# Kernel tuning notes

Measured on AMD Instinct MI355X. Metric: run time of the kernel, lower is better.

The kernel has to match this reference:

```python
import jax, jax.numpy as jnp
import numpy as np

B, T, C, H, N = 4, 4096, 2048, 32, 64
DMIX, DDEC = 32, 64
N_LAYER, LAYER_ID = 24, 12
GN_EPS = 1e-5 * 8.0 ** 2  # eps = 1e-5 * head_size_divisor**2


def setup_inputs() -> dict:
    key = jax.random.key(0)
    ks = jax.random.split(key, 24)
    r01 = LAYER_ID / (N_LAYER - 1)
    r1a0 = 1.0 - LAYER_ID / N_LAYER
    ddd = (np.arange(C, dtype=np.float32) / C).reshape(1, 1, C)
    maa = lambda p: jnp.asarray(1.0 - ddd ** p, dtype=jnp.float32)
    # decay speed schedule (canonical RWKV6, over channel dim)
    n = np.arange(C, dtype=np.float32)
    decay = (-6.0 + 5.0 * (n / (C - 1)) ** (0.7 + 1.3 * r01)).reshape(1, 1, C)
    # time_faaaa zigzag schedule
    m = np.arange(C, dtype=np.float32)
    zig = ((m + 1) % 3 - 1) * 0.1
    faaaa = (r01 * (1 - m / (C - 1)) + zig).reshape(H, N)
    s = 1.0 / np.sqrt(C)
    return {
        "x": jax.random.normal(ks[0], (B, T, C), jnp.float32),
        "shift_state": jax.random.normal(ks[1], (B, C), jnp.float32),
        "wkv_state": jnp.zeros((B, H, N, N), jnp.float32),
        "time_maa_x": maa(r1a0),
        "time_maa_w": maa(r1a0),
        "time_maa_k": maa(r1a0),
        "time_maa_v": jnp.asarray(1.0 - (ddd ** r1a0 + 0.3 * r01), jnp.float32),
        "time_maa_r": maa(0.5 * r1a0),
        "time_maa_g": maa(0.5 * r1a0),
        "time_maa_w1": jax.random.normal(ks[2], (C, 5 * DMIX), jnp.float32) * 0.01,
        "time_maa_w2": jax.random.uniform(ks[3], (5, DMIX, C), jnp.float32, -0.01, 0.01),
        "time_decay": jnp.asarray(decay, jnp.float32),
        "time_decay_w1": jax.random.normal(ks[4], (C, DDEC), jnp.float32) * 0.01,
        "time_decay_w2": jax.random.uniform(ks[5], (DDEC, C), jnp.float32, -0.01, 0.01),
        "time_faaaa": jnp.asarray(faaaa, jnp.float32),
        "Wr": jax.random.normal(ks[6], (C, C), jnp.float32) * s,
        "Wk": jax.random.normal(ks[7], (C, C), jnp.float32) * s,
        "Wv": jax.random.normal(ks[8], (C, C), jnp.float32) * s,
        "Wg": jax.random.normal(ks[9], (C, C), jnp.float32) * s,
        "Wo": jax.random.normal(ks[10], (C, C), jnp.float32) * s,
        "gn_weight": jnp.ones((C,), jnp.float32),
        "gn_bias": jnp.zeros((C,), jnp.float32),
    }


def reference(x, shift_state, wkv_state, time_maa_x, time_maa_w, time_maa_k,
              time_maa_v, time_maa_r, time_maa_g, time_maa_w1, time_maa_w2,
              time_decay, time_decay_w1, time_decay_w2, time_faaaa,
              Wr, Wk, Wv, Wg, Wo, gn_weight, gn_bias):
    b, t, c = x.shape
    # token shift: previous token (seeded by shift_state) minus current
    xx = jnp.concatenate([shift_state[:, None, :], x[:, :-1]], axis=1) - x
    lx = x[:, -1]
    # LoRA token-shift mixing
    xxx = x + xx * time_maa_x
    t5 = jnp.tanh(xxx @ time_maa_w1).reshape(b, t, 5, DMIX)
    mixes = jnp.einsum('btfd,fdc->fbtc', t5, time_maa_w2)
    mw, mk, mv, mr, mg = mixes
    xw = x + xx * (time_maa_w + mw)
    xk = x + xx * (time_maa_k + mk)
    xv = x + xx * (time_maa_v + mv)
    xr = x + xx * (time_maa_r + mr)
    xg = x + xx * (time_maa_g + mg)
    r = xr @ Wr
    k = xk @ Wk
    v = xv @ Wv
    g = jax.nn.silu(xg @ Wg)
    # data-dependent decay via LoRA; wkv6 uses log-decay -exp(w)
    w = time_decay + jnp.tanh(xw @ time_decay_w1) @ time_decay_w2
    glog = -jnp.exp(w)  # [b,t,c]
    to_heads = lambda z: z.reshape(b, t, H, N).transpose(1, 0, 2, 3)  # [t,b,h,n]
    rh, kh, vh, gh = to_heads(r), to_heads(k), to_heads(v), to_heads(glog)
    u = time_faaaa  # [H,N]

    def step(S, inp):
        r_t, k_t, v_t, g_t = inp  # each [b,h,n]
        kv = jnp.einsum('bhk,bhv->bhkv', k_t, v_t)
        o_t = jnp.einsum('bhk,bhkv->bhv', r_t, S + u[None, :, :, None] * kv)
        S = jnp.exp(g_t)[..., None] * S + kv
        return S, o_t

    state, o = jax.lax.scan(step, wkv_state, (rh, kh, vh, gh))
    o = o.transpose(1, 0, 2, 3).reshape(b, t, c)  # [b,t,c]
    # GroupNorm with H groups over channel dim
    og = o.reshape(b, t, H, N)
    mu = og.mean(-1, keepdims=True)
    var = og.var(-1, keepdims=True)
    on = (og - mu) * jax.lax.rsqrt(var + GN_EPS)
    on = on * gn_weight.reshape(H, N) + gn_bias.reshape(H, N)
    out = (on.reshape(b, t, c) * g) @ Wo
    return out, lx, state
```

## Files before the change

### kernel.cpp

```cpp
#include <hip/hip_runtime.h>
#include <hip/hip_bf16.h>
#include <stdint.h>

#define DEV __device__ __forceinline__

typedef __bf16 bf16x8 __attribute__((ext_vector_type(8)));
typedef float f32x4 __attribute__((ext_vector_type(4)));
typedef unsigned short u16x8 __attribute__((ext_vector_type(8)));

constexpr int kB = 4, kT = 4096, kC = 2048, kH = 32, kN = 64;
constexpr int kM = kB * kT;
constexpr int SEGN = 8, TSEG = kT / SEGN, CHN = TSEG / 64;

DEV float bfu2f(unsigned short u) {
  union { uint32_t i; float f; } x; x.i = ((uint32_t)u) << 16; return x.f;
}
DEV unsigned short f2bfu(float f) {
  union { float f; uint32_t i; } x; x.f = f;
  uint32_t r = x.i + 0x7FFFu + ((x.i >> 16) & 1u);
  return (unsigned short)(r >> 16);
}

DEV void gld16(const void* g, void* l) {
  __builtin_amdgcn_global_load_lds(
      (const __attribute__((address_space(1))) void*)g,
      (__attribute__((address_space(3))) void*)l, 16, 0, 0);
}

DEV int swzb(int row, int byteoff) { return (row << 7) + (byteoff ^ ((row & 7) << 4)); }

__global__ __launch_bounds__(256) void trans_bf16(
    const float* __restrict__ in, unsigned short* __restrict__ out, int R, int Cn) {
  __shared__ __attribute__((aligned(16))) unsigned short tile[64][65];
  const int t = threadIdx.x;
  const int r0 = blockIdx.y * 64, c0 = blockIdx.x * 64;
  const int lr = t >> 6, lc = t & 63;
#pragma unroll
  for (int i = 0; i < 16; i++) {
    int rr = lr + i * 4;
    int gr = r0 + rr, gc = c0 + lc;
    if (gr < R && gc < Cn) tile[rr][lc] = f2bfu(in[(size_t)gr * Cn + gc]);
  }
  __syncthreads();
#pragma unroll
  for (int i = 0; i < 16; i++) {
    int cc = lr + i * 4;
    int gc = c0 + cc, gr = r0 + lc;
    if (gc < Cn && gr < R) out[(size_t)gc * R + gr] = tile[lc][cc];
  }
}

__global__ __launch_bounds__(256) void prep_x2(
    const float* __restrict__ x, const float* __restrict__ shift,
    const float* __restrict__ maax,
    unsigned short* __restrict__ xxx, float* __restrict__ lx) {
  size_t i4 = ((size_t)blockIdx.x * 256 + threadIdx.x) * 4;
  int c = (int)(i4 & (kC - 1));
  size_t bt = i4 >> 11;
  int tt = (int)(bt & (kT - 1));
  int b = (int)(bt >> 12);
  float4 xv = *(const float4*)(x + i4);
  float4 pv = (tt == 0) ? *(const float4*)(shift + (size_t)b * kC + c)
                        : *(const float4*)(x + i4 - kC);
  float4 mx = *(const float4*)(maax + c);
  ushort4 o4;
  o4.x = f2bfu(xv.x + (pv.x - xv.x) * mx.x);
  o4.y = f2bfu(xv.y + (pv.y - xv.y) * mx.y);
  o4.z = f2bfu(xv.z + (pv.z - xv.z) * mx.z);
  o4.w = f2bfu(xv.w + (pv.w - xv.w) * mx.w);
  *(ushort4*)(xxx + i4) = o4;
  if (tt == kT - 1) *(float4*)(lx + (size_t)b * kC + c) = xv;
}

enum { E_F32 = 0, E_BF16 = 1, E_TANH = 2, E_SILU = 3, E_DECAY = 4 };

template <int BM, int BN, int EPI>
__global__ __launch_bounds__(256) void gemm_k(
    const unsigned short* __restrict__ A, const unsigned short* __restrict__ Bt,
    void* __restrict__ Cout, const float* __restrict__ aux, int M, int N, int K) {
  constexpr int WGM = (BM == 128 && BN == 128) ? 2 : (BM == 64 ? 2 : 4);
  constexpr int WGN = 4 / WGM;
  constexpr int WM = BM / WGM, WN = BN / WGN;
  constexpr int WR = WM / 16, WC = WN / 16;
  __shared__ __attribute__((aligned(16))) unsigned short As[BM * 32];
  __shared__ __attribute__((aligned(16))) unsigned short Bs[BN * 32];
  const int t = threadIdx.x, wid = t >> 6, l = t & 63;
  const int m0 = blockIdx.x * BM, n0 = blockIdx.y * BN;
  const int wm0 = (wid / WGN) * WM, wn0 = (wid % WGN) * WN;
  f32x4 acc[WR][WC];
#pragma unroll
  for (int i = 0; i < WR; i++)
#pragma unroll
    for (int j = 0; j < WC; j++) acc[i][j] = f32x4{0.f, 0.f, 0.f, 0.f};

  const int rowS = t >> 2, cbS = (t & 3) * 16;
  const char* Ab = (const char*)A;
  const char* Bb = (const char*)Bt;
  const int aoff = (wm0 + (l & 15)) * 32 + (l >> 4) * 8;
  const int boff = (wn0 + (l & 15)) * 32 + (l >> 4) * 8;

  for (int kt = 0; kt < K; kt += 32) {
#pragma unroll
    for (int ia = 0; ia < BM / 64; ia++)
      gld16(Ab + ((size_t)(m0 + ia * 64 + rowS) * K + kt) * 2 + cbS,
            (char*)As + ia * 4096 + wid * 1024);
    if constexpr (BN >= 64) {
#pragma unroll
      for (int ib = 0; ib < BN / 64; ib++)
        gld16(Bb + ((size_t)(n0 + ib * 64 + rowS) * K + kt) * 2 + cbS,
              (char*)Bs + ib * 4096 + wid * 1024);
    } else {
      if (t < BN * 4)
        gld16(Bb + ((size_t)(n0 + rowS) * K + kt) * 2 + cbS,
              (char*)Bs + wid * 1024);
    }
    __syncthreads();
    bf16x8 af[WR], bfv[WC];
#pragma unroll
    for (int mi = 0; mi < WR; mi++) af[mi] = *(const bf16x8*)(&As[aoff + mi * 512]);
#pragma unroll
    for (int ni = 0; ni < WC; ni++) bfv[ni] = *(const bf16x8*)(&Bs[boff + ni * 512]);
#pragma unroll
    for (int mi = 0; mi < WR; mi++)
#pragma unroll
      for (int ni = 0; ni < WC; ni++)
        acc[mi][ni] = __builtin_amdgcn_mfma_f32_16x16x32_bf16(af[mi], bfv[ni], acc[mi][ni], 0, 0, 0);
    __syncthreads();
  }

#pragma unroll
  for (int mi = 0; mi < WR; mi++) {
#pragma unroll
    for (int ni = 0; ni < WC; ni++) {
      int row = m0 + wm0 + mi * 16 + (l >> 4) * 4;
      int col = n0 + wn0 + ni * 16 + (l & 15);
#pragma unroll
      for (int j = 0; j < 4; j++) {
        float v = acc[mi][ni][j];
        size_t idx = (size_t)(row + j) * N + col;
        if constexpr (EPI == E_F32) ((float*)Cout)[idx] = v;
        else if constexpr (EPI == E_BF16) ((unsigned short*)Cout)[idx] = f2bfu(v);
        else if constexpr (EPI == E_TANH) ((unsigned short*)Cout)[idx] = f2bfu(tanhf(v));
        else if constexpr (EPI == E_SILU) ((unsigned short*)Cout)[idx] = f2bfu(v / (1.f + expf(-v)));
        else if constexpr (EPI == E_DECAY) {
          float w = v + aux[col];
          ((float*)Cout)[idx] = expf(-expf(w));
        }
      }
    }
  }
}

DEV void stage256(const unsigned short* A, const unsigned short* Bt,
                  char* lds, int aoff, int boff, int m0, int n0, int K, int kt,
                  int tid, int wid) {
#pragma unroll
  for (int i = 0; i < 4; i++) {
    int row = i * 64 + (tid >> 3);
    int cb = ((tid & 7) * 16) ^ ((row & 7) << 4);
    gld16((const char*)A + ((size_t)(m0 + row) * K + kt) * 2 + cb,
          lds + aoff + i * 8192 + wid * 1024);
    gld16((const char*)Bt + ((size_t)(n0 + row) * K + kt) * 2 + cb,
          lds + boff + i * 8192 + wid * 1024);
  }
}

template <int EPI>
__global__ __launch_bounds__(512, 2) void gemm256_k(
    const unsigned short* __restrict__ A, const unsigned short* __restrict__ Bt,
    void* __restrict__ Cout, int M, int N, int K) {
  extern __shared__ __attribute__((aligned(16))) char lds[];
  const int tid = threadIdx.x, wid = tid >> 6, l = tid & 63;

  const int nwg = gridDim.x, cpx = nwg >> 3;
  int swz = (blockIdx.x & 7) * cpx + (blockIdx.x >> 3);
  const int mtiles = M >> 8;
  const int m0 = (swz % mtiles) * 256, n0 = (swz / mtiles) * 256;

  const int wm = (wid >> 2) * 128, wn = (wid & 3) * 64;
  f32x4 acc[8][4];
#pragma unroll
  for (int i = 0; i < 8; i++)
#pragma unroll
    for (int j = 0; j < 4; j++) acc[i][j] = f32x4{0.f, 0.f, 0.f, 0.f};

  const int KT = K >> 6;
  stage256(A, Bt, lds, 0, 65536, m0, n0, K, 0, tid, wid);
  int cur = 0;

  for (int t = 0; t < KT - 1; ++t) {
    stage256(A, Bt, lds, (cur ^ 1) * 32768, 65536 + (cur ^ 1) * 32768,
             m0, n0, K, (t + 1) * 64, tid, wid);
    asm volatile("s_waitcnt vmcnt(8)" ::: "memory");
    __builtin_amdgcn_s_barrier();
    __builtin_amdgcn_sched_barrier(0);
    {
      const char* Ab = lds + cur * 32768;
      const char* Bb = lds + 65536 + cur * 32768;
      __builtin_amdgcn_s_setprio(1);
#pragma unroll
      for (int ks = 0; ks < 2; ks++) {
        bf16x8 a[8];
#pragma unroll
        for (int mi = 0; mi < 8; mi++)
          a[mi] = *(const bf16x8*)(Ab + swzb(wm + mi * 16 + (l & 15), ks * 64 + (l >> 4) * 16));
#pragma unroll
        for (int ni = 0; ni < 4; ni++) {
          bf16x8 b = *(const bf16x8*)(Bb + swzb(wn + ni * 16 + (l & 15), ks * 64 + (l >> 4) * 16));
#pragma unroll
          for (int mi = 0; mi < 8; mi++)
            acc[mi][ni] = __builtin_amdgcn_mfma_f32_16x16x32_bf16(a[mi], b, acc[mi][ni], 0, 0, 0);
        }
      }
      __builtin_amdgcn_s_setprio(0);
    }
    asm volatile("s_waitcnt lgkmcnt(0)" ::: "memory");
    __builtin_amdgcn_s_barrier();
    __builtin_amdgcn_sched_barrier(0);
    cur ^= 1;
  }

  asm volatile("s_waitcnt vmcnt(0)" ::: "memory");
  __builtin_amdgcn_s_barrier();
  __builtin_amdgcn_sched_barrier(0);
  {
    const char* Ab = lds + cur * 32768;
    const char* Bb = lds + 65536 + cur * 32768;
#pragma unroll
    for (int ks = 0; ks < 2; ks++) {
      bf16x8 a[8];
#pragma unroll
      for (int mi = 0; mi < 8; mi++)
        a[mi] = *(const bf16x8*)(Ab + swzb(wm + mi * 16 + (l & 15), ks * 64 + (l >> 4) * 16));
#pragma unroll
      for (int ni = 0; ni < 4; ni++) {
        bf16x8 b = *(const bf16x8*)(Bb + swzb(wn + ni * 16 + (l & 15), ks * 64 + (l >> 4) * 16));
#pragma unroll
        for (int mi = 0; mi < 8; mi++)
          acc[mi][ni] = __builtin_amdgcn_mfma_f32_16x16x32_bf16(a[mi], b, acc[mi][ni], 0, 0, 0);
      }
    }
  }

#pragma unroll
  for (int mi = 0; mi < 8; mi++)
#pragma unroll
    for (int ni = 0; ni < 4; ni++) {
      int row = m0 + wm + mi * 16 + (l >> 4) * 4;
      int col = n0 + wn + ni * 16 + (l & 15);
#pragma unroll
      for (int j = 0; j < 4; j++) {
        float v = acc[mi][ni][j];
        size_t idx = (size_t)(row + j) * N + col;
        if constexpr (EPI == E_F32) ((float*)Cout)[idx] = v;
        else if constexpr (EPI == E_BF16) ((unsigned short*)Cout)[idx] = f2bfu(v);
        else if constexpr (EPI == E_SILU) ((unsigned short*)Cout)[idx] = f2bfu(v / (1.f + expf(-v)));
      }
    }
}

__global__ __launch_bounds__(256) void mixf_k(
    const unsigned short* __restrict__ t5, const unsigned short* __restrict__ w2t,
    const float* __restrict__ x, const float* __restrict__ shift,
    const float* __restrict__ maa, unsigned short* __restrict__ xout, int f) {
  __shared__ __attribute__((aligned(16))) unsigned short As[64 * 32];
  __shared__ __attribute__((aligned(16))) unsigned short Bs[64 * 32];
  const int t = threadIdx.x, wid = t >> 6, l = t & 63;
  const int m0 = blockIdx.x * 64, n0 = blockIdx.y * 64;
  const int wm0 = (wid >> 1) * 32, wn0 = (wid & 1) * 32;
  const int rowS = t >> 2, cbS = (t & 3) * 16;
  const int aoff = (wm0 + (l & 15)) * 32 + (l >> 4) * 8;
  const int boff = (wn0 + (l & 15)) * 32 + (l >> 4) * 8;

  gld16((const char*)t5 + ((size_t)(m0 + rowS) * 160 + f * 32) * 2 + cbS, (char*)As + wid * 1024);
  gld16((const char*)w2t + ((size_t)(n0 + rowS) * 160 + f * 32) * 2 + cbS, (char*)Bs + wid * 1024);
  __syncthreads();
  bf16x8 a0 = *(const bf16x8*)(&As[aoff]), a1 = *(const bf16x8*)(&As[aoff + 512]);
  bf16x8 b0 = *(const bf16x8*)(&Bs[boff]), b1 = *(const bf16x8*)(&Bs[boff + 512]);
  f32x4 acc[2][2];
  acc[0][0] = f32x4{0.f, 0.f, 0.f, 0.f}; acc[0][1] = f32x4{0.f, 0.f, 0.f, 0.f};
  acc[1][0] = f32x4{0.f, 0.f, 0.f, 0.f}; acc[1][1] = f32x4{0.f, 0.f, 0.f, 0.f};
  acc[0][0] = __builtin_amdgcn_mfma_f32_16x16x32_bf16(a0, b0, acc[0][0], 0, 0, 0);
  acc[0][1] = __builtin_amdgcn_mfma_f32_16x16x32_bf16(a0, b1, acc[0][1], 0, 0, 0);
  acc[1][0] = __builtin_amdgcn_mfma_f32_16x16x32_bf16(a1, b0, acc[1][0], 0, 0, 0);
  acc[1][1] = __builtin_amdgcn_mfma_f32_16x16x32_bf16(a1, b1, acc[1][1], 0, 0, 0);

#pragma unroll
  for (int mi = 0; mi < 2; mi++)
#pragma unroll
    for (int ni = 0; ni < 2; ni++) {
      int row = m0 + wm0 + mi * 16 + (l >> 4) * 4;
      int col = n0 + wn0 + ni * 16 + (l & 15);
      float mv = maa[col];
#pragma unroll
      for (int j = 0; j < 4; j++) {
        int rrow = row + j;
        int tt = rrow & (kT - 1);
        size_t idx = (size_t)rrow * kC + col;
        float xv = x[idx];
        float pv = (tt == 0) ? shift[(size_t)(rrow >> 12) * kC + col] : x[idx - kC];
        xout[idx] = f2bfu(xv + (pv - xv) * (mv + acc[mi][ni][j]));
      }
    }
}

__global__ __launch_bounds__(256) void wkv_local_k(
    const unsigned short* __restrict__ kb, const unsigned short* __restrict__ vb,
    const float* __restrict__ ed, float* __restrict__ Lbuf, float* __restrict__ Dseg) {
  const int bid = blockIdx.x;
  const int bh = bid >> 3, seg = bid & 7;
  const int h = bh & 31, b = bh >> 5;
  const int tid = threadIdx.x, w = tid >> 6, l = tid & 63;
  __shared__ __attribute__((aligned(16))) unsigned short KQks[4096];
  __shared__ __attribute__((aligned(16))) unsigned short Vt[4096];
  __shared__ float segp[4][64];
  __shared__ float DLs[64];

  const int fr = l & 15, fq = l >> 4;
  f32x4 Sreg[4];
#pragma unroll
  for (int ni = 0; ni < 4; ni++) Sreg[ni] = f32x4{0.f, 0.f, 0.f, 0.f};

  float dtot = 1.f;
  float kv[16], dv[16], vv[16];
  {
    size_t g = ((size_t)b * kT + seg * TSEG + w * 16) * kC + h * 64 + l;
#pragma unroll
    for (int i = 0; i < 16; i++) {
      kv[i] = bfu2f(kb[g]); vv[i] = bfu2f(vb[g]); dv[i] = ed[g];
      g += kC;
    }
  }

  for (int ch = 0; ch < CHN; ++ch) {
    float p = 1.f;
#pragma unroll
    for (int i = 0; i < 16; i++) p *= dv[i];
    segp[w][l] = p;
    __syncthreads();
    float pre = 1.f;
    if (w > 0) pre *= segp[0][l];
    if (w > 1) pre *= segp[1][l];
    if (w > 2) pre *= segp[2][l];
    if (w == 3) DLs[l] = pre * p;

    unsigned short kqrow[16], vtrow[16];
    float run = pre;
#pragma unroll
    for (int i = 0; i < 16; i++) {
      run *= dv[i];
      kqrow[i] = f2bfu(kv[i] / run);
      vtrow[i] = f2bfu(vv[i]);
    }
    {
      u16x8 q0, q1, v0, v1;
#pragma unroll
      for (int j = 0; j < 8; j++) { q0[j] = kqrow[j]; q1[j] = kqrow[j + 8]; v0[j] = vtrow[j]; v1[j] = vtrow[j + 8]; }
      *(u16x8*)((char*)KQks + swzb(l, w * 32)) = q0;
      *(u16x8*)((char*)KQks + swzb(l, w * 32 + 16)) = q1;
      *(u16x8*)((char*)Vt + swzb(l, w * 32)) = v0;
      *(u16x8*)((char*)Vt + swzb(l, w * 32 + 16)) = v1;
    }
    if (ch < CHN - 1) {
      size_t g = ((size_t)b * kT + seg * TSEG + (ch + 1) * 64 + w * 16) * kC + h * 64 + l;
#pragma unroll
      for (int i = 0; i < 16; i++) {
        kv[i] = bfu2f(kb[g]); vv[i] = bfu2f(vb[g]); dv[i] = ed[g];
        g += kC;
      }
    }
    __syncthreads();

    bf16x8 kA0 = *(const bf16x8*)((const char*)KQks + swzb(w * 16 + fr, fq * 16));
    bf16x8 kA1 = *(const bf16x8*)((const char*)KQks + swzb(w * 16 + fr, fq * 16 + 64));
    f32x4 kvacc[4];
#pragma unroll
    for (int ni = 0; ni < 4; ni++) {
      bf16x8 bv0 = *(const bf16x8*)((const char*)Vt + swzb(ni * 16 + fr, fq * 16));
      bf16x8 bv1 = *(const bf16x8*)((const char*)Vt + swzb(ni * 16 + fr, fq * 16 + 64));
      kvacc[ni] = __builtin_amdgcn_mfma_f32_16x16x32_bf16(kA0, bv0, f32x4{0.f, 0.f, 0.f, 0.f}, 0, 0, 0);
      kvacc[ni] = __builtin_amdgcn_mfma_f32_16x16x32_bf16(kA1, bv1, kvacc[ni], 0, 0, 0);
    }
    float dlj[4];
#pragma unroll
    for (int j = 0; j < 4; j++) dlj[j] = DLs[w * 16 + fq * 4 + j];
#pragma unroll
    for (int ni = 0; ni < 4; ni++)
#pragma unroll
      for (int j = 0; j < 4; j++)
        Sreg[ni][j] = (Sreg[ni][j] + kvacc[ni][j]) * dlj[j];
    dtot *= DLs[l];
    __syncthreads();
  }

  float* Lp = Lbuf + (size_t)bid * 4096;
#pragma unroll
  for (int ni = 0; ni < 4; ni++)
#pragma unroll
    for (int j = 0; j < 4; j++)
      Lp[(size_t)(w * 16 + fq * 4 + j) * 64 + ni * 16 + fr] = Sreg[ni][j];
  if (w == 0) Dseg[(size_t)bid * 64 + l] = dtot;
}

__global__ __launch_bounds__(256) void wkv_combine_k(
    const float* __restrict__ s0, const float* __restrict__ Dseg,
    float* __restrict__ Lbuf, float* __restrict__ sOut) {
  const int bh = blockIdx.x, tid = threadIdx.x;
  const int k = tid >> 2, v0 = (tid & 3) * 16;
  float4 s[4];
  const float* sp = s0 + (size_t)bh * 4096 + (size_t)k * 64 + v0;
#pragma unroll
  for (int q = 0; q < 4; q++) s[q] = ((const float4*)sp)[q];
  for (int seg = 0; seg < SEGN; ++seg) {
    size_t idx = (size_t)bh * SEGN + seg;
    float d = Dseg[idx * 64 + k];
    float* Lp = Lbuf + idx * 4096 + (size_t)k * 64 + v0;
#pragma unroll
    for (int q = 0; q < 4; q++) {
      float4 lq = ((float4*)Lp)[q];
      ((float4*)Lp)[q] = s[q];
      s[q].x = d * s[q].x + lq.x; s[q].y = d * s[q].y + lq.y;
      s[q].z = d * s[q].z + lq.z; s[q].w = d * s[q].w + lq.w;
    }
  }
  float* op = sOut + (size_t)bh * 4096 + (size_t)k * 64 + v0;
#pragma unroll
  for (int q = 0; q < 4; q++) ((float4*)op)[q] = s[q];
}

__global__ __launch_bounds__(256) void wkv_seg_k(
    const unsigned short* __restrict__ rb, const unsigned short* __restrict__ kb,
    const unsigned short* __restrict__ vb, const float* __restrict__ ed,
    const float* __restrict__ uf, const float* __restrict__ Sini,
    unsigned short* __restrict__ o) {
  const int bid = blockIdx.x;
  const int bh = bid >> 3, seg = bid & 7;
  const int h = bh & 31, b = bh >> 5;
  const int tid = threadIdx.x, w = tid >> 6, l = tid & 63;
  __shared__ __attribute__((aligned(16))) unsigned short RQ[4096];
  __shared__ __attribute__((aligned(16))) unsigned short KQsk[4096];
  __shared__ __attribute__((aligned(16))) unsigned short KQks[4096];
  __shared__ __attribute__((aligned(16))) unsigned short Vt[4096];
  __shared__ __attribute__((aligned(16))) unsigned short Pl[4096];
  __shared__ __attribute__((aligned(16))) unsigned short S0T[4096];
  __shared__ __attribute__((aligned(16))) unsigned short RU[4096];
  __shared__ __attribute__((aligned(16))) unsigned short Ksk[4096];
  __shared__ float segp[4][64];
  __shared__ float DLs[64];

  const float uu = uf[h * 64 + l];
  const int fr = l & 15, fq = l >> 4;

  f32x4 Sreg[4];
#pragma unroll
  for (int ni = 0; ni < 4; ni++)
#pragma unroll
    for (int j = 0; j < 4; j++) {
      int kk2 = w * 16 + fq * 4 + j, vv2 = ni * 16 + fr;
      float sv = Sini[(size_t)bid * 4096 + (size_t)kk2 * 64 + vv2];
      Sreg[ni][j] = sv;
      *(unsigned short*)((char*)S0T + swzb(vv2, kk2 * 2)) = f2bfu(sv);
    }
  __syncthreads();

  float rv[16], kv[16], dv[16], vv[16];
  {
    size_t g = ((size_t)b * kT + seg * TSEG + w * 16) * kC + h * 64 + l;
#pragma unroll
    for (int i = 0; i < 16; i++) {
      rv[i] = bfu2f(rb[g]); kv[i] = bfu2f(kb[g]); vv[i] = bfu2f(vb[g]); dv[i] = ed[g];
      g += kC;
    }
  }

  for (int ch = 0; ch < CHN; ++ch) {
    float p = 1.f;
#pragma unroll
    for (int i = 0; i < 16; i++) p *= dv[i];
    segp[w][l] = p;
    __syncthreads();
    float pre = 1.f;
    if (w > 0) pre *= segp[0][l];
    if (w > 1) pre *= segp[1][l];
    if (w > 2) pre *= segp[2][l];
    if (w == 3) DLs[l] = pre * p;

    unsigned short kqrow[16], vtrow[16];
    float run = pre;
#pragma unroll
    for (int i = 0; i < 16; i++) {
      int t = w * 16 + i;
      float rq = rv[i] * run;
      run *= dv[i];
      float kq = kv[i] / run;
      *(unsigned short*)((char*)RQ + swzb(t, l * 2)) = f2bfu(rq);
      *(unsigned short*)((char*)RU + swzb(t, l * 2)) = f2bfu(rv[i] * uu);
      *(unsigned short*)((char*)Ksk + swzb(t, l * 2)) = f2bfu(kv[i]);
      unsigned short kqu = f2bfu(kq);
      *(unsigned short*)((char*)KQsk + swzb(t, l * 2)) = kqu;
      kqrow[i] = kqu;
      vtrow[i] = f2bfu(vv[i]);
    }
    {
      u16x8 q0, q1, v0, v1;
#pragma unroll
      for (int j = 0; j < 8; j++) { q0[j] = kqrow[j]; q1[j] = kqrow[j + 8]; v0[j] = vtrow[j]; v1[j] = vtrow[j + 8]; }
      *(u16x8*)((char*)KQks + swzb(l, w * 32)) = q0;
      *(u16x8*)((char*)KQks + swzb(l, w * 32 + 16)) = q1;
      *(u16x8*)((char*)Vt + swzb(l, w * 32)) = v0;
      *(u16x8*)((char*)Vt + swzb(l, w * 32 + 16)) = v1;
    }

    if (ch < CHN - 1) {
      size_t g = ((size_t)b * kT + seg * TSEG + (ch + 1) * 64 + w * 16) * kC + h * 64 + l;
#pragma unroll
      for (int i = 0; i < 16; i++) {
        rv[i] = bfu2f(rb[g]); kv[i] = bfu2f(kb[g]); vv[i] = bfu2f(vb[g]); dv[i] = ed[g];
        g += kC;
      }
    }
    __syncthreads();

    bf16x8 a0 = *(const bf16x8*)((const char*)RQ + swzb(w * 16 + fr, fq * 16));
    bf16x8 a1 = *(const bf16x8*)((const char*)RQ + swzb(w * 16 + fr, fq * 16 + 64));
    f32x4 pacc[4];
#pragma unroll
    for (int ni = 0; ni < 4; ni++) {
      bf16x8 b0 = *(const bf16x8*)((const char*)KQsk + swzb(ni * 16 + fr, fq * 16));
      bf16x8 b1 = *(const bf16x8*)((const char*)KQsk + swzb(ni * 16 + fr, fq * 16 + 64));
      pacc[ni] = __builtin_amdgcn_mfma_f32_16x16x32_bf16(a0, b0, f32x4{0.f, 0.f, 0.f, 0.f}, 0, 0, 0);
      pacc[ni] = __builtin_amdgcn_mfma_f32_16x16x32_bf16(a1, b1, pacc[ni], 0, 0, 0);
    }
    f32x4 dacc;
    {
      bf16x8 ru0 = *(const bf16x8*)((const char*)RU + swzb(w * 16 + fr, fq * 16));
      bf16x8 ru1 = *(const bf16x8*)((const char*)RU + swzb(w * 16 + fr, fq * 16 + 64));
      bf16x8 kb0 = *(const bf16x8*)((const char*)Ksk + swzb(w * 16 + fr, fq * 16));
      bf16x8 kb1 = *(const bf16x8*)((const char*)Ksk + swzb(w * 16 + fr, fq * 16 + 64));
      dacc = __builtin_amdgcn_mfma_f32_16x16x32_bf16(ru0, kb0, f32x4{0.f, 0.f, 0.f, 0.f}, 0, 0, 0);
      dacc = __builtin_amdgcn_mfma_f32_16x16x32_bf16(ru1, kb1, dacc, 0, 0, 0);
    }
    float dg[4];
#pragma unroll
    for (int j = 0; j < 4; j++) dg[j] = __shfl(dacc[j], fq * 20 + j, 64);
#pragma unroll
    for (int ni = 0; ni < 4; ni++)
#pragma unroll
      for (int j = 0; j < 4; j++) {
        int row = w * 16 + fq * 4 + j, col = ni * 16 + fr;
        float pv = pacc[ni][j];
        pv = (col < row) ? pv : ((col == row) ? dg[j] : 0.f);
        *(unsigned short*)((char*)Pl + swzb(row, col * 2)) = f2bfu(pv);
      }
    __syncthreads();

    bf16x8 pA0 = *(const bf16x8*)((const char*)Pl + swzb(w * 16 + fr, fq * 16));
    bf16x8 pA1 = *(const bf16x8*)((const char*)Pl + swzb(w * 16 + fr, fq * 16 + 64));
    bf16x8 kA0 = *(const bf16x8*)((const char*)KQks + swzb(w * 16 + fr, fq * 16));
    bf16x8 kA1 = *(const bf16x8*)((const char*)KQks + swzb(w * 16 + fr, fq * 16 + 64));
    f32x4 oacc[4], kvacc[4];
#pragma unroll
    for (int ni = 0; ni < 4; ni++) {
      bf16x8 bv0 = *(const bf16x8*)((const char*)Vt + swzb(ni * 16 + fr, fq * 16));
      bf16x8 bv1 = *(const bf16x8*)((const char*)Vt + swzb(ni * 16 + fr, fq * 16 + 64));
      bf16x8 bs0 = *(const bf16x8*)((const char*)S0T + swzb(ni * 16 + fr, fq * 16));
      bf16x8 bs1 = *(const bf16x8*)((const char*)S0T + swzb(ni * 16 + fr, fq * 16 + 64));
      oacc[ni] = __builtin_amdgcn_mfma_f32_16x16x32_bf16(pA0, bv0, f32x4{0.f, 0.f, 0.f, 0.f}, 0, 0, 0);
      oacc[ni] = __builtin_amdgcn_mfma_f32_16x16x32_bf16(pA1, bv1, oacc[ni], 0, 0, 0);
      oacc[ni] = __builtin_amdgcn_mfma_f32_16x16x32_bf16(a0, bs0, oacc[ni], 0, 0, 0);
      oacc[ni] = __builtin_amdgcn_mfma_f32_16x16x32_bf16(a1, bs1, oacc[ni], 0, 0, 0);
      kvacc[ni] = __builtin_amdgcn_mfma_f32_16x16x32_bf16(kA0, bv0, f32x4{0.f, 0.f, 0.f, 0.f}, 0, 0, 0);
      kvacc[ni] = __builtin_amdgcn_mfma_f32_16x16x32_bf16(kA1, bv1, kvacc[ni], 0, 0, 0);
    }
    size_t obase = ((size_t)b * kT + seg * TSEG + ch * 64) * kC + h * 64;
#pragma unroll
    for (int ni = 0; ni < 4; ni++)
#pragma unroll
      for (int j = 0; j < 4; j++)
        o[obase + (size_t)(w * 16 + fq * 4 + j) * kC + ni * 16 + fr] = f2bfu(oacc[ni][j]);
    __syncthreads();

    float dlj[4];
#pragma unroll
    for (int j = 0; j < 4; j++) dlj[j] = DLs[w * 16 + fq * 4 + j];
#pragma unroll
    for (int ni = 0; ni < 4; ni++)
#pragma unroll
      for (int j = 0; j < 4; j++) {
        int kk2 = w * 16 + fq * 4 + j, vv2 = ni * 16 + fr;
        float sn = (Sreg[ni][j] + kvacc[ni][j]) * dlj[j];
        Sreg[ni][j] = sn;
        *(unsigned short*)((char*)S0T + swzb(vv2, kk2 * 2)) = f2bfu(sn);
      }
    __syncthreads();
  }
}

__global__ __launch_bounds__(256) void gn_k(
    const unsigned short* __restrict__ o, const unsigned short* __restrict__ gb,
    const float* __restrict__ gnw, const float* __restrict__ gnb,
    unsigned short* __restrict__ y) {
  int gi = blockIdx.x * 4 + (threadIdx.x >> 6);
  int j = threadIdx.x & 63;
  int bt = gi >> 5, h = gi & 31;
  size_t idx = (size_t)bt * kC + h * 64 + j;
  float val = bfu2f(o[idx]);
  float s = val, s2 = val * val;
#pragma unroll
  for (int m = 1; m < 64; m <<= 1) {
    s += __shfl_xor(s, m, 64);
    s2 += __shfl_xor(s2, m, 64);
  }
  float mu = s * 0.015625f;
  float var = s2 * 0.015625f - mu * mu;
  float rs = rsqrtf(var + 6.4e-4f);
  float on = (val - mu) * rs * gnw[h * 64 + j] + gnb[h * 64 + j];
  y[idx] = f2bfu(on * bfu2f(gb[idx]));
}

constexpr size_t SZW     = (size_t)2048 * 2048 * 2;
constexpr size_t OFF_WRT = 0;
constexpr size_t OFF_WKT = 1 * SZW;
constexpr size_t OFF_WVT = 2 * SZW;
constexpr size_t OFF_WGT = 3 * SZW;
constexpr size_t OFF_WOT = 4 * SZW;
constexpr size_t OFF_W1T = 5 * SZW;
constexpr size_t OFF_W2T = OFF_W1T + (size_t)160 * 2048 * 2;
constexpr size_t OFF_TD1 = OFF_W2T + (size_t)2048 * 160 * 2;
constexpr size_t OFF_TD2 = OFF_TD1 + (size_t)64 * 2048 * 2;
constexpr size_t OFF_T5  = OFF_TD2 + (size_t)2048 * 64 * 2;
constexpr size_t OFF_DT  = OFF_T5 + (size_t)kM * 160 * 2;
constexpr size_t OFF_EDEC= OFF_DT + (size_t)kM * 64 * 2;
constexpr size_t OFF_XMIX= OFF_EDEC + (size_t)kM * kC * 4;
constexpr size_t OFF_R   = OFF_XMIX + (size_t)kM * kC * 2;
constexpr size_t OFF_K   = OFF_R + (size_t)kM * kC * 2;
constexpr size_t OFF_V   = OFF_K + (size_t)kM * kC * 2;
constexpr size_t OFF_L   = OFF_WRT;

extern "C" void kernel_launch(void* const* d_in, const int* in_sizes, int n_in,
                              void* d_out, int out_size, void* d_ws, size_t ws_size,
                              hipStream_t stream) {
  const float* x     = (const float*)d_in[0];
  const float* shift = (const float*)d_in[1];
  const float* s0    = (const float*)d_in[2];
  const float* maax  = (const float*)d_in[3];
  const float* maaw  = (const float*)d_in[4];
  const float* maak  = (const float*)d_in[5];
  const float* maav  = (const float*)d_in[6];
  const float* maar  = (const float*)d_in[7];
  const float* maag  = (const float*)d_in[8];
  const float* w1    = (const float*)d_in[9];
  const float* w2    = (const float*)d_in[10];
  const float* tdec  = (const float*)d_in[11];
  const float* tdw1  = (const float*)d_in[12];
  const float* tdw2  = (const float*)d_in[13];
  const float* faaaa = (const float*)d_in[14];
  const float* Wr    = (const float*)d_in[15];
  const float* Wk    = (const float*)d_in[16];
  const float* Wv    = (const float*)d_in[17];
  const float* Wg    = (const float*)d_in[18];
  const float* Wo    = (const float*)d_in[19];
  const float* gnw   = (const float*)d_in[20];
  const float* gnb   = (const float*)d_in[21];

  char* ws = (char*)d_ws;
  unsigned short* Wrt  = (unsigned short*)(ws + OFF_WRT);
  unsigned short* Wkt  = (unsigned short*)(ws + OFF_WKT);
  unsigned short* Wvt  = (unsigned short*)(ws + OFF_WVT);
  unsigned short* Wgt  = (unsigned short*)(ws + OFF_WGT);
  unsigned short* Wot  = (unsigned short*)(ws + OFF_WOT);
  unsigned short* w1t  = (unsigned short*)(ws + OFF_W1T);
  unsigned short* w2t  = (unsigned short*)(ws + OFF_W2T);
  unsigned short* td1t = (unsigned short*)(ws + OFF_TD1);
  unsigned short* td2t = (unsigned short*)(ws + OFF_TD2);
  unsigned short* t5   = (unsigned short*)(ws + OFF_T5);
  unsigned short* dtmp = (unsigned short*)(ws + OFF_DT);
  float*          edec = (float*)(ws + OFF_EDEC);
  unsigned short* xg   = (unsigned short*)(ws + OFF_EDEC);
  unsigned short* xmix = (unsigned short*)(ws + OFF_XMIX);
  unsigned short* obf  = (unsigned short*)(ws + OFF_XMIX);
  unsigned short* rbb  = (unsigned short*)(ws + OFF_R);
  unsigned short* gbb  = (unsigned short*)(ws + OFF_R);
  unsigned short* kbb  = (unsigned short*)(ws + OFF_K);
  unsigned short* ybuf = (unsigned short*)(ws + OFF_K);
  unsigned short* vbb  = (unsigned short*)(ws + OFF_V);
  float*          Lbuf = (float*)(ws + OFF_L);
  float*          DsegP= (float*)(ws + OFF_TD1);

  float* outp  = (float*)d_out;
  float* lx    = outp + (size_t)kM * kC;
  float* stOut = lx + (size_t)kB * kC;

  dim3 blk(256);

  trans_bf16<<<dim3(32, 32), blk, 0, stream>>>(Wr, Wrt, 2048, 2048);
  trans_bf16<<<dim3(32, 32), blk, 0, stream>>>(Wk, Wkt, 2048, 2048);
  trans_bf16<<<dim3(32, 32), blk, 0, stream>>>(Wv, Wvt, 2048, 2048);
  trans_bf16<<<dim3(32, 32), blk, 0, stream>>>(Wg, Wgt, 2048, 2048);
  trans_bf16<<<dim3(32, 32), blk, 0, stream>>>(Wo, Wot, 2048, 2048);
  trans_bf16<<<dim3(3, 32), blk, 0, stream>>>(w1, w1t, 2048, 160);
  trans_bf16<<<dim3(1, 32), blk, 0, stream>>>(tdw1, td1t, 2048, 64);
  trans_bf16<<<dim3(32, 1), blk, 0, stream>>>(tdw2, td2t, 64, 2048);
  trans_bf16<<<dim3(32, 3), blk, 0, stream>>>(w2, w2t, 160, 2048);

  prep_x2<<<dim3(kM * kC / 4 / 256), blk, 0, stream>>>(x, shift, maax, xmix, lx);

  gemm_k<128, 32, E_TANH><<<dim3(kM / 128, 5), blk, 0, stream>>>(xmix, w1t, t5, nullptr, kM, 160, 2048);

  dim3 mgrid(kM / 64, kC / 64);
  constexpr int G256 = (kM / 256) * (kC / 256);
  constexpr size_t LDS256 = 131072;

  mixf_k<<<mgrid, blk, 0, stream>>>(t5, w2t, x, shift, maaw, xmix, 0);
  gemm_k<64, 64, E_TANH><<<dim3(kM / 64, 1), blk, 0, stream>>>(xmix, td1t, dtmp, nullptr, kM, 64, 2048);
  gemm_k<128, 128, E_DECAY><<<dim3(kM / 128, 16), blk, 0, stream>>>(dtmp, td2t, edec, tdec, kM, 2048, 64);

  mixf_k<<<mgrid, blk, 0, stream>>>(t5, w2t, x, shift, maak, xmix, 1);
  gemm256_k<E_BF16><<<dim3(G256), dim3(512), LDS256, stream>>>(xmix, Wkt, kbb, kM, 2048, 2048);
  mixf_k<<<mgrid, blk, 0, stream>>>(t5, w2t, x, shift, maav, xmix, 2);
  gemm256_k<E_BF16><<<dim3(G256), dim3(512), LDS256, stream>>>(xmix, Wvt, vbb, kM, 2048, 2048);
  mixf_k<<<mgrid, blk, 0, stream>>>(t5, w2t, x, shift, maar, xmix, 3);
  gemm256_k<E_BF16><<<dim3(G256), dim3(512), LDS256, stream>>>(xmix, Wrt, rbb, kM, 2048, 2048);

  wkv_local_k<<<dim3(kB * kH * SEGN), blk, 0, stream>>>(kbb, vbb, edec, Lbuf, DsegP);
  wkv_combine_k<<<dim3(kB * kH), blk, 0, stream>>>(s0, DsegP, Lbuf, stOut);
  wkv_seg_k<<<dim3(kB * kH * SEGN), blk, 0, stream>>>(rbb, kbb, vbb, edec, faaaa, Lbuf, obf);

  mixf_k<<<mgrid, blk, 0, stream>>>(t5, w2t, x, shift, maag, xg, 4);
  gemm256_k<E_SILU><<<dim3(G256), dim3(512), LDS256, stream>>>(xg, Wgt, gbb, kM, 2048, 2048);

  gn_k<<<dim3(kM * kH / 4), blk, 0, stream>>>(obf, gbb, gnw, gnb, ybuf);

  gemm256_k<E_F32><<<dim3(G256), dim3(512), LDS256, stream>>>(ybuf, Wot, outp, kM, 2048, 2048);
}
```

Baseline: 1.577 ms.

## Prefetch GEMM tiles two stages ahead, remap XCD tiles, fuse paired mix kernels

The 256x256 GEMM now issues the load for tile t+2 after the post-compute barrier instead of loading t+1 at the start of each iteration. This gives each global load more time to land before it is needed. Block-to-tile mapping is changed so each XCD owns a contiguous M slab covering all N tiles, which should improve L2 reuse of A rows. A new mix2f_k computes two token-shift mix outputs per launch, sharing the x and shift reads, and buffers are reassigned so the k/v/r inputs can coexist. This needs an extra bf16 buffer alive at once and relies on a careful buffer aliasing order.

```diff
diff --git a/kernel.cpp b/kernel.cpp
--- a/kernel.cpp
+++ b/kernel.cpp
@@ -172,10 +172,11 @@
   extern __shared__ __attribute__((aligned(16))) char lds[];
   const int tid = threadIdx.x, wid = tid >> 6, l = tid & 63;
 
-  const int nwg = gridDim.x, cpx = nwg >> 3;
-  int swz = (blockIdx.x & 7) * cpx + (blockIdx.x >> 3);
-  const int mtiles = M >> 8;
-  const int m0 = (swz % mtiles) * 256, n0 = (swz / mtiles) * 256;
+  const int mtiles = M >> 8, ntiles = N >> 8;
+  const int slab = mtiles >> 3;
+  const int xcd = blockIdx.x & 7, loc = blockIdx.x >> 3;
+  const int m0 = (xcd * slab + loc / ntiles) * 256;
+  const int n0 = (loc % ntiles) * 256;
 
   const int wm = (wid >> 2) * 128, wn = (wid & 3) * 64;
   f32x4 acc[8][4];
@@ -186,11 +187,10 @@
 
   const int KT = K >> 6;
   stage256(A, Bt, lds, 0, 65536, m0, n0, K, 0, tid, wid);
+  stage256(A, Bt, lds, 32768, 65536 + 32768, m0, n0, K, 64, tid, wid);
   int cur = 0;
 
   for (int t = 0; t < KT - 1; ++t) {
-    stage256(A, Bt, lds, (cur ^ 1) * 32768, 65536 + (cur ^ 1) * 32768,
-             m0, n0, K, (t + 1) * 64, tid, wid);
     asm volatile("s_waitcnt vmcnt(8)" ::: "memory");
     __builtin_amdgcn_s_barrier();
     __builtin_amdgcn_sched_barrier(0);
@@ -217,6 +217,9 @@
     asm volatile("s_waitcnt lgkmcnt(0)" ::: "memory");
     __builtin_amdgcn_s_barrier();
     __builtin_amdgcn_sched_barrier(0);
+    if (t + 2 < KT)
+      stage256(A, Bt, lds, cur * 32768, 65536 + cur * 32768,
+               m0, n0, K, (t + 2) * 64, tid, wid);
     cur ^= 1;
   }
 
@@ -255,6 +258,67 @@
         if constexpr (EPI == E_F32) ((float*)Cout)[idx] = v;
         else if constexpr (EPI == E_BF16) ((unsigned short*)Cout)[idx] = f2bfu(v);
         else if constexpr (EPI == E_SILU) ((unsigned short*)Cout)[idx] = f2bfu(v / (1.f + expf(-v)));
+      }
+    }
+}
+
+__global__ __launch_bounds__(256) void mix2f_k(
+    const unsigned short* __restrict__ t5, const unsigned short* __restrict__ w2t,
+    const float* __restrict__ x, const float* __restrict__ shift,
+    const float* __restrict__ maa1, const float* __restrict__ maa2,
+    unsigned short* __restrict__ xo1, unsigned short* __restrict__ xo2,
+    int f1, int f2) {
+  __shared__ __attribute__((aligned(16))) unsigned short As1[64 * 32];
+  __shared__ __attribute__((aligned(16))) unsigned short Bs1[64 * 32];
+  __shared__ __attribute__((aligned(16))) unsigned short As2[64 * 32];
+  __shared__ __attribute__((aligned(16))) unsigned short Bs2[64 * 32];
+  const int t = threadIdx.x, wid = t >> 6, l = t & 63;
+  const int m0 = blockIdx.x * 64, n0 = blockIdx.y * 64;
+  const int wm0 = (wid >> 1) * 32, wn0 = (wid & 1) * 32;
+  const int rowS = t >> 2, cbS = (t & 3) * 16;
+  const int aoff = (wm0 + (l & 15)) * 32 + (l >> 4) * 8;
+  const int boff = (wn0 + (l & 15)) * 32 + (l >> 4) * 8;
+
+  gld16((const char*)t5 + ((size_t)(m0 + rowS) * 160 + f1 * 32) * 2 + cbS, (char*)As1 + wid * 1024);
+  gld16((const char*)w2t + ((size_t)(n0 + rowS) * 160 + f1 * 32) * 2 + cbS, (char*)Bs1 + wid * 1024);
+  gld16((const char*)t5 + ((size_t)(m0 + rowS) * 160 + f2 * 32) * 2 + cbS, (char*)As2 + wid * 1024);
+  gld16((const char*)w2t + ((size_t)(n0 + rowS) * 160 + f2 * 32) * 2 + cbS, (char*)Bs2 + wid * 1024);
+  __syncthreads();
+  bf16x8 a10 = *(const bf16x8*)(&As1[aoff]), a11 = *(const bf16x8*)(&As1[aoff + 512]);
+  bf16x8 b10 = *(const bf16x8*)(&Bs1[boff]), b11 = *(const bf16x8*)(&Bs1[boff + 512]);
+  bf16x8 a20 = *(const bf16x8*)(&As2[aoff]), a21 = *(const bf16x8*)(&As2[aoff + 512]);
+  bf16x8 b20 = *(const bf16x8*)(&Bs2[boff]), b21 = *(const bf16x8*)(&Bs2[boff + 512]);
+  f32x4 ac1[2][2], ac2[2][2];
+#pragma unroll
+  for (int i = 0; i < 2; i++)
+#pragma unroll
+    for (int j = 0; j < 2; j++) { ac1[i][j] = f32x4{0.f, 0.f, 0.f, 0.f}; ac2[i][j] = f32x4{0.f, 0.f, 0.f, 0.f}; }
+  ac1[0][0] = __builtin_amdgcn_mfma_f32_16x16x32_bf16(a10, b10, ac1[0][0], 0, 0, 0);
+  ac1[0][1] = __builtin_amdgcn_mfma_f32_16x16x32_bf16(a10, b11, ac1[0][1], 0, 0, 0);
+  ac1[1][0] = __builtin_amdgcn_mfma_f32_16x16x32_bf16(a11, b10, ac1[1][0], 0, 0, 0);
+  ac1[1][1] = __builtin_amdgcn_mfma_f32_16x16x32_bf16(a11, b11, ac1[1][1], 0, 0, 0);
+  ac2[0][0] = __builtin_amdgcn_mfma_f32_16x16x32_bf16(a20, b20, ac2[0][0], 0, 0, 0);
+  ac2[0][1] = __builtin_amdgcn_mfma_f32_16x16x32_bf16(a20, b21, ac2[0][1], 0, 0, 0);
+  ac2[1][0] = __builtin_amdgcn_mfma_f32_16x16x32_bf16(a21, b20, ac2[1][0], 0, 0, 0);
+  ac2[1][1] = __builtin_amdgcn_mfma_f32_16x16x32_bf16(a21, b21, ac2[1][1], 0, 0, 0);
+
+#pragma unroll
+  for (int mi = 0; mi < 2; mi++)
+#pragma unroll
+    for (int ni = 0; ni < 2; ni++) {
+      int row = m0 + wm0 + mi * 16 + (l >> 4) * 4;
+      int col = n0 + wn0 + ni * 16 + (l & 15);
+      float mv1 = maa1[col], mv2 = maa2[col];
+#pragma unroll
+      for (int j = 0; j < 4; j++) {
+        int rrow = row + j;
+        int tt = rrow & (kT - 1);
+        size_t idx = (size_t)rrow * kC + col;
+        float xv = x[idx];
+        float pv = (tt == 0) ? shift[(size_t)(rrow >> 12) * kC + col] : x[idx - kC];
+        float d = pv - xv;
+        xo1[idx] = f2bfu(xv + d * (mv1 + ac1[mi][ni][j]));
+        xo2[idx] = f2bfu(xv + d * (mv2 + ac2[mi][ni][j]));
       }
     }
 }
@@ -677,13 +741,10 @@
   unsigned short* dtmp = (unsigned short*)(ws + OFF_DT);
   float*          edec = (float*)(ws + OFF_EDEC);
   unsigned short* xg   = (unsigned short*)(ws + OFF_EDEC);
-  unsigned short* xmix = (unsigned short*)(ws + OFF_XMIX);
-  unsigned short* obf  = (unsigned short*)(ws + OFF_XMIX);
-  unsigned short* rbb  = (unsigned short*)(ws + OFF_R);
-  unsigned short* gbb  = (unsigned short*)(ws + OFF_R);
-  unsigned short* kbb  = (unsigned short*)(ws + OFF_K);
-  unsigned short* ybuf = (unsigned short*)(ws + OFF_K);
-  unsigned short* vbb  = (unsigned short*)(ws + OFF_V);
+  unsigned short* bufX = (unsigned short*)(ws + OFF_XMIX);
+  unsigned short* bufR = (unsigned short*)(ws + OFF_R);
+  unsigned short* bufK = (unsigned short*)(ws + OFF_K);
+  unsigned short* bufV = (unsigned short*)(ws + OFF_V);
   float*          Lbuf = (float*)(ws + OFF_L);
   float*          DsegP= (float*)(ws + OFF_TD1);
 
@@ -703,33 +764,31 @@
   trans_bf16<<<dim3(32, 1), blk, 0, stream>>>(tdw2, td2t, 64, 2048);
   trans_bf16<<<dim3(32, 3), blk, 0, stream>>>(w2, w2t, 160, 2048);
 
-  prep_x2<<<dim3(kM * kC / 4 / 256), blk, 0, stream>>>(x, shift, maax, xmix, lx);
-
-  gemm_k<128, 32, E_TANH><<<dim3(kM / 128, 5), blk, 0, stream>>>(xmix, w1t, t5, nullptr, kM, 160, 2048);
+  prep_x2<<<dim3(kM * kC / 4 / 256), blk, 0, stream>>>(x, shift, maax, bufX, lx);
+
+  gemm_k<128, 32, E_TANH><<<dim3(kM / 128, 5), blk, 0, stream>>>(bufX, w1t, t5, nullptr, kM, 160, 2048);
 
   dim3 mgrid(kM / 64, kC / 64);
   constexpr int G256 = (kM / 256) * (kC / 256);
   constexpr size_t LDS256 = 131072;
 
-  mixf_k<<<mgrid, blk, 0, stream>>>(t5, w2t, x, shift, maaw, xmix, 0);
-  gemm_k<64, 64, E_TANH><<<dim3(kM / 64, 1), blk, 0, stream>>>(xmix, td1t, dtmp, nullptr, kM, 64, 2048);
+  mix2f_k<<<mgrid, blk, 0, stream>>>(t5, w2t, x, shift, maaw, maak, bufX, bufV, 0, 1);
+  gemm_k<64, 64, E_TANH><<<dim3(kM / 64, 1), blk, 0, stream>>>(bufX, td1t, dtmp, nullptr, kM, 64, 2048);
   gemm_k<128, 128, E_DECAY><<<dim3(kM / 128, 16), blk, 0, stream>>>(dtmp, td2t, edec, tdec, kM, 2048, 64);
-
-  mixf_k<<<mgrid, blk, 0, stream>>>(t5, w2t, x, shift, maak, xmix, 1);
-  gemm256_k<E_BF16><<<dim3(G256), dim3(512), LDS256, stream>>>(xmix, Wkt, kbb, kM, 2048, 2048);
-  mixf_k<<<mgrid, blk, 0, stream>>>(t5, w2t, x, shift, maav, xmix, 2);
-  gemm256_k<E_BF16><<<dim3(G256), dim3(512), LDS256, stream>>>(xmix, Wvt, vbb, kM, 2048, 2048);
-  mixf_k<<<mgrid, blk, 0, stream>>>(t5, w2t, x, shift, maar, xmix, 3);
-  gemm256_k<E_BF16><<<dim3(G256), dim3(512), LDS256, stream>>>(xmix, Wrt, rbb, kM, 2048, 2048);
-
-  wkv_local_k<<<dim3(kB * kH * SEGN), blk, 0, stream>>>(kbb, vbb, edec, Lbuf, DsegP);
+  gemm256_k<E_BF16><<<dim3(G256), dim3(512), LDS256, stream>>>(bufV, Wkt, bufK, kM, 2048, 2048);
+
+  mix2f_k<<<mgrid, blk, 0, stream>>>(t5, w2t, x, shift, maav, maar, bufX, bufV, 2, 3);
+  gemm256_k<E_BF16><<<dim3(G256), dim3(512), LDS256, stream>>>(bufX, Wvt, bufR, kM, 2048, 2048);
+  gemm256_k<E_BF16><<<dim3(G256), dim3(512), LDS256, stream>>>(bufV, Wrt, bufX, kM, 2048, 2048);
+
+  wkv_local_k<<<dim3(kB * kH * SEGN), blk, 0, stream>>>(bufK, bufR, edec, Lbuf, DsegP);
   wkv_combine_k<<<dim3(kB * kH), blk, 0, stream>>>(s0, DsegP, Lbuf, stOut);
-  wkv_seg_k<<<dim3(kB * kH * SEGN), blk, 0, stream>>>(rbb, kbb, vbb, edec, faaaa, Lbuf, obf);
+  wkv_seg_k<<<dim3(kB * kH * SEGN), blk, 0, stream>>>(bufX, bufK, bufR, edec, faaaa, Lbuf, bufV);
 
   mixf_k<<<mgrid, blk, 0, stream>>>(t5, w2t, x, shift, maag, xg, 4);
-  gemm256_k<E_SILU><<<dim3(G256), dim3(512), LDS256, stream>>>(xg, Wgt, gbb, kM, 2048, 2048);
-
-  gn_k<<<dim3(kM * kH / 4), blk, 0, stream>>>(obf, gbb, gnw, gnb, ybuf);
-
-  gemm256_k<E_F32><<<dim3(G256), dim3(512), LDS256, stream>>>(ybuf, Wot, outp, kM, 2048, 2048);
-}
+  gemm256_k<E_SILU><<<dim3(G256), dim3(512), LDS256, stream>>>(xg, Wgt, bufK, kM, 2048, 2048);
+
+  gn_k<<<dim3(kM * kH / 4), blk, 0, stream>>>(bufV, bufK, gnw, gnb, bufR);
+
+  gemm256_k<E_F32><<<dim3(G256), dim3(512), LDS256, stream>>>(bufR, Wot, outp, kM, 2048, 2048);
+}
```

After: 1.560 ms. About the same (-1.1%).
